# Kernel optimization log

Measured on AMD Instinct MI355X. Metric: run time of the kernel, lower is better.

Reference implementation:

```python
import jax, jax.numpy as jnp
import numpy as np

BZ, T, D, DFF, E, BEAMS = 128, 32, 768, 3072, 8, 2


def setup_inputs() -> dict:
    key = jax.random.key(0)
    ks = jax.random.split(key, 4)
    s = 0.02
    return {
        "x": jax.random.normal(ks[0], (BZ, T, D), jnp.float32),
        "attention_mask": jnp.ones((BZ, T), jnp.float32),
        "Wg": jax.random.normal(ks[1], (D, E), jnp.float32) * s,   # gate Linear(D,E,bias=False)
        "W1": jax.random.normal(ks[2], (E, D, DFF), jnp.float32) * s,
        "b1": jnp.zeros((E, DFF), jnp.float32),
        "W2": jax.random.normal(ks[3], (E, DFF, D), jnp.float32) * s,
        "b2": jnp.zeros((E, D), jnp.float32),
    }


def reference(x, attention_mask, Wg, W1, b1, W2, b2):
    # forward_gate: module builds its own all-ones mask regardless of input mask
    mask = jnp.ones((x.shape[0], x.shape[1]), x.dtype)
    x_avg = (x * mask[..., None]).sum(1) / mask[..., None].sum(1)   # [bz, D]
    prob = jax.nn.softmax(x_avg @ Wg, axis=-1)                       # [bz, E]
    # beam_search (layer_judge='first', pre-route): topk on exp(log(softmax)) == softmax probs
    scores = jnp.exp(jnp.log(prob))
    topv, topi = jax.lax.top_k(scores, BEAMS)                        # [bz, beams]
    beam_scores = topv.reshape(-1)                                   # [bz*beams]
    expert_route = topi.reshape(-1, 1)                                # [bz*beams, 1]
    sel = expert_route[:, -1]
    # replicate x per beam: [bz*beams, T, D]
    x_rep = jnp.broadcast_to(x[:, None], (x.shape[0], BEAMS, x.shape[1], x.shape[2]))
    x_rep = x_rep.reshape(-1, x.shape[1], x.shape[2])
    # per-sample expert FFN dispatch (dense masked loop over the E=8 experts)
    out = jnp.zeros_like(x_rep)
    for e in range(E):
        h = jax.nn.gelu(jnp.einsum('nsd,df->nsf', x_rep, W1[e]) + b1[e], approximate=False)
        ye = jnp.einsum('nsf,fd->nsd', h, W2[e]) + b2[e]
        out = jnp.where((sel == e)[:, None, None], ye, out)
    return (out, beam_scores, expert_route)
```

## Files before the change

### kernel.cpp

```cpp
#include <hip/hip_runtime.h>
#include <cstddef>
#include <cstdint>

#define BZd   128
#define Td    32
#define Dd    768
#define DFFd  3072
#define Ed    8
#define NBEAM 256
#define ROWS_TOT 8192
#define OUT_ELEMS 6291456
#define MAXTILES 72
#define MAXT2    40

typedef unsigned short u16;
typedef __attribute__((ext_vector_type(4))) unsigned short ushort4v;
typedef __attribute__((ext_vector_type(8))) short frag_ab;
typedef __attribute__((ext_vector_type(4))) float floatx4;

__device__ __forceinline__ u16 f2bf(float f) {
  unsigned int u = __builtin_bit_cast(unsigned int, f);
  u += 0x7FFFu + ((u >> 16) & 1u);
  return (u16)(u >> 16);
}

__device__ __forceinline__ void async_copy16(u16* lds, const u16* g) {
  __builtin_amdgcn_global_load_lds(
      (const __attribute__((address_space(1))) void*)g,
      (__attribute__((address_space(3))) void*)lds, 16, 0, 0);
}

__device__ __forceinline__ float gelu_fast(float x) {
  float z = 1.5957691216f * (x + 0.044715f * x * x * x);
  return x / (1.0f + __expf(-z));
}

__global__ __launch_bounds__(256) void route_kernel(
    const float* __restrict__ x, const float* __restrict__ Wg,
    float* __restrict__ out, int* __restrict__ sel) {
  int b = blockIdx.x;
  int t = threadIdx.x;
  __shared__ float red[256][8];
  float la[8];
#pragma unroll
  for (int e = 0; e < 8; e++) la[e] = 0.f;
  for (int d = t; d < Dd; d += 256) {
    const float* xp = x + (size_t)b * Td * Dd + d;
    float xa = 0.f;
#pragma unroll
    for (int tt = 0; tt < Td; tt++) xa += xp[(size_t)tt * Dd];
    xa *= (1.0f / 32.0f);
#pragma unroll
    for (int e = 0; e < 8; e++) la[e] += xa * Wg[d * 8 + e];
  }
#pragma unroll
  for (int e = 0; e < 8; e++) red[t][e] = la[e];
  __syncthreads();
  for (int s = 128; s > 0; s >>= 1) {
    if (t < s) {
#pragma unroll
      for (int e = 0; e < 8; e++) red[t][e] += red[t + s][e];
    }
    __syncthreads();
  }
  if (t == 0) {
    float lg[8];
#pragma unroll
    for (int e = 0; e < 8; e++) lg[e] = red[0][e];
    float mx = lg[0];
#pragma unroll
    for (int e = 1; e < 8; e++) mx = fmaxf(mx, lg[e]);
    float p[8];
    float sum = 0.f;
#pragma unroll
    for (int e = 0; e < 8; e++) { p[e] = __expf(lg[e] - mx); sum += p[e]; }
    float inv = 1.0f / sum;
#pragma unroll
    for (int e = 0; e < 8; e++) p[e] *= inv;
    int i0 = 0; float v0 = p[0];
#pragma unroll
    for (int e = 1; e < 8; e++) if (p[e] > v0) { v0 = p[e]; i0 = e; }
    int i1 = -1; float v1 = -1.0f;
#pragma unroll
    for (int e = 0; e < 8; e++) if (e != i0 && p[e] > v1) { v1 = p[e]; i1 = e; }
    float* bs = out + OUT_ELEMS;
    float* er = out + OUT_ELEMS + NBEAM;
    bs[2 * b] = v0; bs[2 * b + 1] = v1;
    er[2 * b] = (float)i0; er[2 * b + 1] = (float)i1;
    sel[2 * b] = i0; sel[2 * b + 1] = i1;
  }
}

__global__ __launch_bounds__(256) void bucket_kernel(
    const int* __restrict__ sel, int* __restrict__ perm,
    int4* __restrict__ tiles, int4* __restrict__ tiles2) {
  __shared__ int ssel[NBEAM];
  __shared__ int scnt[8];
  __shared__ int soff[8];
  __shared__ int scur[8];
  __shared__ int sperm[NBEAM];
  int t = threadIdx.x;
  ssel[t] = sel[t];
  __syncthreads();
  if (t == 0) {
    for (int e = 0; e < 8; e++) scnt[e] = 0;
    for (int n = 0; n < NBEAM; n++) scnt[ssel[n]]++;
    int o = 0;
    for (int e = 0; e < 8; e++) { soff[e] = o; scur[e] = o; o += scnt[e]; }
    for (int n = 0; n < NBEAM; n++) { int e = ssel[n]; sperm[scur[e]++] = n; }
    int tt = 0;
    for (int e = 0; e < 8; e++) {
      int nr = scnt[e] * 32;
      int base = soff[e] * 32;
      for (int r0 = 0; r0 < nr; r0 += 128) {
        tiles[tt] = make_int4(e, base + r0, min(128, nr - r0), 0);
        tt++;
      }
    }
    for (; tt < MAXTILES; tt++) tiles[tt] = make_int4(-1, 0, 0, 0);
    int t2 = 0;
    for (int e = 0; e < 8; e++) {
      int nr = scnt[e] * 32;
      int base = soff[e] * 32;
      for (int r0 = 0; r0 < nr; r0 += 256) {
        tiles2[t2] = make_int4(e, base + r0, min(256, nr - r0), 0);
        t2++;
      }
    }
    for (; t2 < MAXT2; t2++) tiles2[t2] = make_int4(-1, 0, 0, 0);
  }
  __syncthreads();
  perm[t] = sperm[t];
}

__global__ __launch_bounds__(256) void convert_x_kernel(
    const float* __restrict__ x, u16* __restrict__ xbf) {
  size_t i = ((size_t)blockIdx.x * 256 + threadIdx.x) * 4;
  float4 v = *(const float4*)(x + i);
  ushort4v pv = {f2bf(v.x), f2bf(v.y), f2bf(v.z), f2bf(v.w)};
  *(ushort4v*)(xbf + i) = pv;
}

__global__ __launch_bounds__(256) void transpose_bf16_kernel(
    const float* __restrict__ in, u16* __restrict__ out, int row0, int col0,
    int ld_in, size_t estr_in, int ld_out, size_t estr_out) {
  __shared__ u16 tile[64][65];
  int e = blockIdx.z;
  int r0 = blockIdx.x * 64, c0 = blockIdx.y * 64;
  int t = threadIdx.x;
  int rr = t >> 4, cc4 = (t & 15) * 4;
  const float* ip = in + (size_t)e * estr_in + (size_t)(row0 + r0) * ld_in + col0 + c0;
#pragma unroll
  for (int i = 0; i < 4; i++) {
    int r = rr + 16 * i;
    float4 v = *(const float4*)(ip + (size_t)r * ld_in + cc4);
    tile[r][cc4 + 0] = f2bf(v.x);
    tile[r][cc4 + 1] = f2bf(v.y);
    tile[r][cc4 + 2] = f2bf(v.z);
    tile[r][cc4 + 3] = f2bf(v.w);
  }
  __syncthreads();
  int ccw = t >> 4, r4 = (t & 15) * 4;
  u16* op = out + (size_t)e * estr_out + (size_t)c0 * ld_out + r0;
#pragma unroll
  for (int i = 0; i < 4; i++) {
    int cc = ccw + 16 * i;
    ushort4v pv = {tile[r4 + 0][cc], tile[r4 + 1][cc], tile[r4 + 2][cc], tile[r4 + 3][cc]};
    *(ushort4v*)(op + (size_t)cc * ld_out + r4) = pv;
  }
}

__global__ __launch_bounds__(512, 2) void gemm1_kernel(
    const u16* __restrict__ xbf, const u16* __restrict__ w1t,
    const float* __restrict__ b1, const int* __restrict__ perm,
    const int4* __restrict__ tiles2, u16* __restrict__ h, int f0, int FC) {
  int4 meta = tiles2[blockIdx.y];
  int e = meta.x;
  if (e < 0) return;
  int grow0 = meta.y, nrows = meta.z;
  int bx = blockIdx.x;

  extern __shared__ __align__(16) u16 smem[];
  u16* As = smem;
  u16* Bs = smem + 32768;

  int t = threadIdx.x;
  int l = t & 63;
  int wid = t >> 6;
  int wr = wid >> 2;
  int wc = wid & 3;
  int lrow = l & 15, lquad = l >> 4;

  const u16* ag[4]; const u16* bg[4];
  int ldst[4];
#pragma unroll
  for (int j = 0; j < 4; j++) {
    int s = j * 512 + t;
    int m = s >> 3;
    int koff = ((s & 7) ^ ((m >> 1) & 7)) * 8;
    int gr = grow0 + m;
    int bidx = gr >> 5; bidx = bidx < NBEAM ? bidx : NBEAM - 1;
    int batch = perm[bidx] >> 1;
    ag[j] = xbf + ((size_t)batch * Td + (m & 31)) * Dd + koff;
    bg[j] = w1t + ((size_t)e * FC + bx * 256 + m) * Dd + koff;
    ldst[j] = j * 4096 + t * 8;
  }

  int swz = (lrow >> 1) & 7;
  int ca0 = (lquad ^ swz) * 8, ca1 = ((lquad + 4) ^ swz) * 8;
  int abase0 = (wr * 128 + lrow) * 64 + ca0;
  int abase1 = (wr * 128 + lrow) * 64 + ca1;
  int bbase0 = (wc * 64 + lrow) * 64 + ca0;
  int bbase1 = (wc * 64 + lrow) * 64 + ca1;

  floatx4 acc[8][4];
#pragma unroll
  for (int mi = 0; mi < 8; mi++)
#pragma unroll
    for (int ni = 0; ni < 4; ni++) acc[mi][ni] = (floatx4){0.f, 0.f, 0.f, 0.f};

  const int nk = Dd / 64;

#pragma unroll
  for (int j = 0; j < 4; j++) { async_copy16(As + ldst[j], ag[j]); ag[j] += 64; }
#pragma unroll
  for (int j = 0; j < 4; j++) { async_copy16(Bs + ldst[j], bg[j]); bg[j] += 64; }

  for (int kt = 0; kt < nk; kt++) {
    const int b = kt & 1;
    const u16* Ab = As + b * 16384;
    const u16* Bb = Bs + b * 16384;
    const int pd = (b ^ 1) * 16384;
    const bool pre = (kt + 1 < nk);

    frag_ab af[4], bfr[4];

    if (pre) {
      async_copy16(As + pd + ldst[0], ag[0]); ag[0] += 64;
      async_copy16(As + pd + ldst[1], ag[1]); ag[1] += 64;
      asm volatile("s_waitcnt vmcnt(2)\n\ts_barrier" ::: "memory");
    } else {
      asm volatile("s_waitcnt vmcnt(0)\n\ts_barrier" ::: "memory");
    }
#pragma unroll
    for (int i = 0; i < 4; i++) bfr[i] = *(const frag_ab*)(Bb + bbase0 + i * 1024);
#pragma unroll
    for (int i = 0; i < 4; i++) af[i] = *(const frag_ab*)(Ab + abase0 + i * 1024);
    __builtin_amdgcn_s_setprio(1);
#pragma unroll
    for (int mi = 0; mi < 4; mi++)
#pragma unroll
      for (int ni = 0; ni < 4; ni++)
        acc[mi][ni] = __builtin_amdgcn_mfma_f32_16x16x32_bf16(bfr[ni], af[mi], acc[mi][ni], 0, 0, 0);
    __builtin_amdgcn_s_setprio(0);

    if (pre) {
      async_copy16(As + pd + ldst[2], ag[2]); ag[2] += 64;
      async_copy16(As + pd + ldst[3], ag[3]); ag[3] += 64;
    }
#pragma unroll
    for (int i = 0; i < 4; i++) af[i] = *(const frag_ab*)(Ab + abase0 + (i + 4) * 1024);
    __builtin_amdgcn_s_setprio(1);
#pragma unroll
    for (int mi = 0; mi < 4; mi++)
#pragma unroll
      for (int ni = 0; ni < 4; ni++)
        acc[mi + 4][ni] = __builtin_amdgcn_mfma_f32_16x16x32_bf16(bfr[ni], af[mi], acc[mi + 4][ni], 0, 0, 0);
    __builtin_amdgcn_s_setprio(0);

    if (pre) {
      async_copy16(Bs + pd + ldst[0], bg[0]); bg[0] += 64;
      async_copy16(Bs + pd + ldst[1], bg[1]); bg[1] += 64;
    }
#pragma unroll
    for (int i = 0; i < 4; i++) bfr[i] = *(const frag_ab*)(Bb + bbase1 + i * 1024);
#pragma unroll
    for (int i = 0; i < 4; i++) af[i] = *(const frag_ab*)(Ab + abase1 + i * 1024);
    __builtin_amdgcn_s_setprio(1);
#pragma unroll
    for (int mi = 0; mi < 4; mi++)
#pragma unroll
      for (int ni = 0; ni < 4; ni++)
        acc[mi][ni] = __builtin_amdgcn_mfma_f32_16x16x32_bf16(bfr[ni], af[mi], acc[mi][ni], 0, 0, 0);
    __builtin_amdgcn_s_setprio(0);

    if (pre) {
      async_copy16(Bs + pd + ldst[2], bg[2]); bg[2] += 64;
      async_copy16(Bs + pd + ldst[3], bg[3]); bg[3] += 64;
    }
#pragma unroll
    for (int i = 0; i < 4; i++) af[i] = *(const frag_ab*)(Ab + abase1 + (i + 4) * 1024);
    __builtin_amdgcn_s_setprio(1);
#pragma unroll
    for (int mi = 0; mi < 4; mi++)
#pragma unroll
      for (int ni = 0; ni < 4; ni++)
        acc[mi + 4][ni] = __builtin_amdgcn_mfma_f32_16x16x32_bf16(bfr[ni], af[mi], acc[mi + 4][ni], 0, 0, 0);
    __builtin_amdgcn_s_setprio(0);

    asm volatile("s_barrier" ::: "memory");
  }

#pragma unroll
  for (int mi = 0; mi < 8; mi++) {
    int row = wr * 128 + mi * 16 + lrow;
    if (row < nrows) {
      u16* hp = h + (size_t)(grow0 + row) * FC + bx * 256 + wc * 64 + lquad * 4;
      const float* bp = b1 + (size_t)e * DFFd + f0 + bx * 256 + wc * 64 + lquad * 4;
#pragma unroll
      for (int ni = 0; ni < 4; ni++) {
        float4 bias = *(const float4*)(bp + ni * 16);
        ushort4v pv = {f2bf(gelu_fast(acc[mi][ni][0] + bias.x)),
                       f2bf(gelu_fast(acc[mi][ni][1] + bias.y)),
                       f2bf(gelu_fast(acc[mi][ni][2] + bias.z)),
                       f2bf(gelu_fast(acc[mi][ni][3] + bias.w))};
        *(ushort4v*)(hp + ni * 16) = pv;
      }
    }
  }
}

__global__ __launch_bounds__(512, 2) void gemm2_kernel(
    const u16* __restrict__ h, const u16* __restrict__ w2t,
    const float* __restrict__ b2, const int* __restrict__ perm,
    const int4* __restrict__ tiles2, float* __restrict__ out,
    int FC, int first) {
  int4 meta = tiles2[blockIdx.y];
  int e = meta.x;
  if (e < 0) return;
  int grow0 = meta.y, nrows = meta.z;
  int bx = blockIdx.x;

  extern __shared__ __align__(16) u16 smem[];
  u16* As = smem;
  u16* Bs = smem + 32768;
  __shared__ int sbeam[8];

  int t = threadIdx.x;
  if (t < 8) {
    int idx = (grow0 >> 5) + t;
    sbeam[t] = perm[idx < NBEAM ? idx : NBEAM - 1];
  }
  __syncthreads();

  int l = t & 63;
  int wid = t >> 6;
  int wr = wid >> 2;
  int wc = wid & 3;
  int lrow = l & 15, lquad = l >> 4;

  const u16* ag[4]; const u16* bg[4];
  int ldst[4];
#pragma unroll
  for (int j = 0; j < 4; j++) {
    int s = j * 512 + t;
    int m = s >> 3;
    int koff = ((s & 7) ^ ((m >> 1) & 7)) * 8;
    int arow = grow0 + m;
    arow = arow < ROWS_TOT ? arow : ROWS_TOT - 1;
    ag[j] = h + (size_t)arow * FC + koff;
    bg[j] = w2t + ((size_t)e * Dd + bx * 256 + m) * FC + koff;
    ldst[j] = j * 4096 + t * 8;
  }

  int swz = (lrow >> 1) & 7;
  int ca0 = (lquad ^ swz) * 8, ca1 = ((lquad + 4) ^ swz) * 8;
  int abase0 = (wr * 128 + lrow) * 64 + ca0;
  int abase1 = (wr * 128 + lrow) * 64 + ca1;
  int bbase0 = (wc * 64 + lrow) * 64 + ca0;
  int bbase1 = (wc * 64 + lrow) * 64 + ca1;

  floatx4 acc[8][4];
#pragma unroll
  for (int mi = 0; mi < 8; mi++)
#pragma unroll
    for (int ni = 0; ni < 4; ni++) acc[mi][ni] = (floatx4){0.f, 0.f, 0.f, 0.f};

  const int nk = FC / 64;

#pragma unroll
  for (int j = 0; j < 4; j++) { async_copy16(As + ldst[j], ag[j]); ag[j] += 64; }
#pragma unroll
  for (int j = 0; j < 4; j++) { async_copy16(Bs + ldst[j], bg[j]); bg[j] += 64; }

  for (int kt = 0; kt < nk; kt++) {
    const int b = kt & 1;
    const u16* Ab = As + b * 16384;
    const u16* Bb = Bs + b * 16384;
    const int pd = (b ^ 1) * 16384;
    const bool pre = (kt + 1 < nk);

    frag_ab af[4], bfr[4];

    if (pre) {
      async_copy16(As + pd + ldst[0], ag[0]); ag[0] += 64;
      async_copy16(As + pd + ldst[1], ag[1]); ag[1] += 64;
      asm volatile("s_waitcnt vmcnt(2)\n\ts_barrier" ::: "memory");
    } else {
      asm volatile("s_waitcnt vmcnt(0)\n\ts_barrier" ::: "memory");
    }
#pragma unroll
    for (int i = 0; i < 4; i++) bfr[i] = *(const frag_ab*)(Bb + bbase0 + i * 1024);
#pragma unroll
    for (int i = 0; i < 4; i++) af[i] = *(const frag_ab*)(Ab + abase0 + i * 1024);
    __builtin_amdgcn_s_setprio(1);
#pragma unroll
    for (int mi = 0; mi < 4; mi++)
#pragma unroll
      for (int ni = 0; ni < 4; ni++)
        acc[mi][ni] = __builtin_amdgcn_mfma_f32_16x16x32_bf16(bfr[ni], af[mi], acc[mi][ni], 0, 0, 0);
    __builtin_amdgcn_s_setprio(0);

    if (pre) {
      async_copy16(As + pd + ldst[2], ag[2]); ag[2] += 64;
      async_copy16(As + pd + ldst[3], ag[3]); ag[3] += 64;
    }
#pragma unroll
    for (int i = 0; i < 4; i++) af[i] = *(const frag_ab*)(Ab + abase0 + (i + 4) * 1024);
    __builtin_amdgcn_s_setprio(1);
#pragma unroll
    for (int mi = 0; mi < 4; mi++)
#pragma unroll
      for (int ni = 0; ni < 4; ni++)
        acc[mi + 4][ni] = __builtin_amdgcn_mfma_f32_16x16x32_bf16(bfr[ni], af[mi], acc[mi + 4][ni], 0, 0, 0);
    __builtin_amdgcn_s_setprio(0);

    if (pre) {
      async_copy16(Bs + pd + ldst[0], bg[0]); bg[0] += 64;
      async_copy16(Bs + pd + ldst[1], bg[1]); bg[1] += 64;
    }
#pragma unroll
    for (int i = 0; i < 4; i++) bfr[i] = *(const frag_ab*)(Bb + bbase1 + i * 1024);
#pragma unroll
    for (int i = 0; i < 4; i++) af[i] = *(const frag_ab*)(Ab + abase1 + i * 1024);
    __builtin_amdgcn_s_setprio(1);
#pragma unroll
    for (int mi = 0; mi < 4; mi++)
#pragma unroll
      for (int ni = 0; ni < 4; ni++)
        acc[mi][ni] = __builtin_amdgcn_mfma_f32_16x16x32_bf16(bfr[ni], af[mi], acc[mi][ni], 0, 0, 0);
    __builtin_amdgcn_s_setprio(0);

    if (pre) {
      async_copy16(Bs + pd + ldst[2], bg[2]); bg[2] += 64;
      async_copy16(Bs + pd + ldst[3], bg[3]); bg[3] += 64;
    }
#pragma unroll
    for (int i = 0; i < 4; i++) af[i] = *(const frag_ab*)(Ab + abase1 + (i + 4) * 1024);
    __builtin_amdgcn_s_setprio(1);
#pragma unroll
    for (int mi = 0; mi < 4; mi++)
#pragma unroll
      for (int ni = 0; ni < 4; ni++)
        acc[mi + 4][ni] = __builtin_amdgcn_mfma_f32_16x16x32_bf16(bfr[ni], af[mi], acc[mi + 4][ni], 0, 0, 0);
    __builtin_amdgcn_s_setprio(0);

    asm volatile("s_barrier" ::: "memory");
  }

#pragma unroll
  for (int mi = 0; mi < 8; mi++) {
    int row = wr * 128 + mi * 16 + lrow;
    if (row < nrows) {
      int beam = sbeam[row >> 5];
      float* op = out + ((size_t)beam * Td + (row & 31)) * Dd + bx * 256 + wc * 64 + lquad * 4;
      const float* bp = b2 + (size_t)e * Dd + bx * 256 + wc * 64 + lquad * 4;
#pragma unroll
      for (int ni = 0; ni < 4; ni++) {
        if (first) {
          float4 bias = *(const float4*)(bp + ni * 16);
          float4 v = {acc[mi][ni][0] + bias.x, acc[mi][ni][1] + bias.y,
                      acc[mi][ni][2] + bias.z, acc[mi][ni][3] + bias.w};
          *(float4*)(op + ni * 16) = v;
        } else {
          float4 o = *(float4*)(op + ni * 16);
          o.x += acc[mi][ni][0]; o.y += acc[mi][ni][1];
          o.z += acc[mi][ni][2]; o.w += acc[mi][ni][3];
          *(float4*)(op + ni * 16) = o;
        }
      }
    }
  }
}

extern "C" void kernel_launch(void* const* d_in, const int* in_sizes, int n_in,
                              void* d_out, int out_size, void* d_ws, size_t ws_size,
                              hipStream_t stream) {
  const float* x  = (const float*)d_in[0];
  const float* Wg = (const float*)d_in[2];
  const float* W1 = (const float*)d_in[3];
  const float* b1 = (const float*)d_in[4];
  const float* W2 = (const float*)d_in[5];
  const float* b2 = (const float*)d_in[6];
  float* out = (float*)d_out;

  char* ws = (char*)d_ws;
  int*  sel    = (int*)ws;
  int*  perm   = sel + NBEAM;
  int4* tiles  = (int4*)(ws + 4096);
  int4* tiles2 = (int4*)(ws + 6144);

  const size_t xbf_off = 65536;
  const size_t xbf_bytes = (size_t)BZd * Td * Dd * 2;
  int FC = 768;
  if      (xbf_off + xbf_bytes + (size_t)40960 * 3072 <= ws_size) FC = 3072;
  else if (xbf_off + xbf_bytes + (size_t)40960 * 1536 <= ws_size) FC = 1536;
  int NC = DFFd / FC;

  u16* xbf = (u16*)(ws + xbf_off);
  u16* w1t = (u16*)(ws + xbf_off + xbf_bytes);
  u16* w2t = w1t + (size_t)Ed * FC * Dd;
  u16* h   = w2t + (size_t)Ed * Dd * FC;

  static bool attr_done = false;
  if (!attr_done) {
    hipFuncSetAttribute(reinterpret_cast<const void*>(gemm1_kernel),
                        hipFuncAttributeMaxDynamicSharedMemorySize, 131072);
    hipFuncSetAttribute(reinterpret_cast<const void*>(gemm2_kernel),
                        hipFuncAttributeMaxDynamicSharedMemorySize, 131072);
    attr_done = true;
  }

  route_kernel<<<BZd, 256, 0, stream>>>(x, Wg, out, sel);
  bucket_kernel<<<1, 256, 0, stream>>>(sel, perm, tiles, tiles2);
  convert_x_kernel<<<(BZd * Td * Dd) / 1024, 256, 0, stream>>>(x, xbf);

  for (int c = 0; c < NC; c++) {
    transpose_bf16_kernel<<<dim3(Dd / 64, FC / 64, Ed), 256, 0, stream>>>(
        W1, w1t, 0, c * FC, DFFd, (size_t)Dd * DFFd, Dd, (size_t)FC * Dd);
    transpose_bf16_kernel<<<dim3(FC / 64, Dd / 64, Ed), 256, 0, stream>>>(
        W2, w2t, c * FC, 0, Dd, (size_t)DFFd * Dd, FC, (size_t)Dd * FC);
    gemm1_kernel<<<dim3(FC / 256, MAXT2), 512, 131072, stream>>>(
        xbf, w1t, b1, perm, tiles2, h, c * FC, FC);
    gemm2_kernel<<<dim3(Dd / 256, MAXT2), 512, 131072, stream>>>(
        h, w2t, b2, perm, tiles2, out, FC, c == 0 ? 1 : 0);
  }
}
```

Before: 377.0 us.

## Split-K gemm2 over two slices with atomic accumulation and bias prefill in routing

Splits the second expert GEMM's reduction dimension into two halves along a new grid z dimension, doubling the number of workgroups, and accumulates results into the output with per-element float atomicAdd. The routing kernel now prefills the output with each beam's selected expert bias b2, so gemm2 no longer needs a first-chunk store path. The aim is to fix under-occupancy of the GPU, since gemm2 previously launched only 3 x 40 blocks. The cost is many scalar atomics to global memory, an extra full-output write in the routing kernel, and a summation order that is no longer deterministic.

```diff
diff --git a/kernel.cpp b/kernel.cpp
--- a/kernel.cpp
+++ b/kernel.cpp
@@ -37,10 +37,12 @@
 
 __global__ __launch_bounds__(256) void route_kernel(
     const float* __restrict__ x, const float* __restrict__ Wg,
-    float* __restrict__ out, int* __restrict__ sel) {
+    const float* __restrict__ b2, float* __restrict__ out,
+    int* __restrict__ sel) {
   int b = blockIdx.x;
   int t = threadIdx.x;
   __shared__ float red[256][8];
+  __shared__ int se2[2];
   float la[8];
 #pragma unroll
   for (int e = 0; e < 8; e++) la[e] = 0.f;
@@ -88,6 +90,17 @@
     bs[2 * b] = v0; bs[2 * b + 1] = v1;
     er[2 * b] = (float)i0; er[2 * b + 1] = (float)i1;
     sel[2 * b] = i0; sel[2 * b + 1] = i1;
+    se2[0] = i0; se2[1] = i1;
+  }
+  __syncthreads();
+#pragma unroll
+  for (int bm = 0; bm < 2; bm++) {
+    const float* brow = b2 + (size_t)se2[bm] * Dd;
+    float* orow = out + (size_t)(2 * b + bm) * Td * Dd;
+    for (int i = t; i < Td * Dd / 4; i += 256) {
+      float4 v = *(const float4*)(brow + (i % (Dd / 4)) * 4);
+      *(float4*)(orow + (size_t)i * 4) = v;
+    }
   }
 }
 
@@ -322,14 +335,15 @@
 
 __global__ __launch_bounds__(512, 2) void gemm2_kernel(
     const u16* __restrict__ h, const u16* __restrict__ w2t,
-    const float* __restrict__ b2, const int* __restrict__ perm,
-    const int4* __restrict__ tiles2, float* __restrict__ out,
-    int FC, int first) {
+    const int* __restrict__ perm, const int4* __restrict__ tiles2,
+    float* __restrict__ out, int FC) {
   int4 meta = tiles2[blockIdx.y];
   int e = meta.x;
   if (e < 0) return;
   int grow0 = meta.y, nrows = meta.z;
   int bx = blockIdx.x;
+  int kz = blockIdx.z;
+  const int KC = FC >> 1;
 
   extern __shared__ __align__(16) u16 smem[];
   u16* As = smem;
@@ -358,8 +372,8 @@
     int koff = ((s & 7) ^ ((m >> 1) & 7)) * 8;
     int arow = grow0 + m;
     arow = arow < ROWS_TOT ? arow : ROWS_TOT - 1;
-    ag[j] = h + (size_t)arow * FC + koff;
-    bg[j] = w2t + ((size_t)e * Dd + bx * 256 + m) * FC + koff;
+    ag[j] = h + (size_t)arow * FC + kz * KC + koff;
+    bg[j] = w2t + ((size_t)e * Dd + bx * 256 + m) * FC + kz * KC + koff;
     ldst[j] = j * 4096 + t * 8;
   }
 
@@ -376,7 +390,7 @@
 #pragma unroll
     for (int ni = 0; ni < 4; ni++) acc[mi][ni] = (floatx4){0.f, 0.f, 0.f, 0.f};
 
-  const int nk = FC / 64;
+  const int nk = KC / 64;
 
 #pragma unroll
   for (int j = 0; j < 4; j++) { async_copy16(As + ldst[j], ag[j]); ag[j] += 64; }
@@ -464,20 +478,11 @@
     if (row < nrows) {
       int beam = sbeam[row >> 5];
       float* op = out + ((size_t)beam * Td + (row & 31)) * Dd + bx * 256 + wc * 64 + lquad * 4;
-      const float* bp = b2 + (size_t)e * Dd + bx * 256 + wc * 64 + lquad * 4;
 #pragma unroll
       for (int ni = 0; ni < 4; ni++) {
-        if (first) {
-          float4 bias = *(const float4*)(bp + ni * 16);
-          float4 v = {acc[mi][ni][0] + bias.x, acc[mi][ni][1] + bias.y,
-                      acc[mi][ni][2] + bias.z, acc[mi][ni][3] + bias.w};
-          *(float4*)(op + ni * 16) = v;
-        } else {
-          float4 o = *(float4*)(op + ni * 16);
-          o.x += acc[mi][ni][0]; o.y += acc[mi][ni][1];
-          o.z += acc[mi][ni][2]; o.w += acc[mi][ni][3];
-          *(float4*)(op + ni * 16) = o;
-        }
+#pragma unroll
+        for (int jj = 0; jj < 4; jj++)
+          atomicAdd(op + ni * 16 + jj, acc[mi][ni][jj]);
       }
     }
   }
@@ -521,7 +526,7 @@
     attr_done = true;
   }
 
-  route_kernel<<<BZd, 256, 0, stream>>>(x, Wg, out, sel);
+  route_kernel<<<BZd, 256, 0, stream>>>(x, Wg, b2, out, sel);
   bucket_kernel<<<1, 256, 0, stream>>>(sel, perm, tiles, tiles2);
   convert_x_kernel<<<(BZd * Td * Dd) / 1024, 256, 0, stream>>>(x, xbf);
 
@@ -532,7 +537,7 @@
         W2, w2t, c * FC, 0, Dd, (size_t)DFFd * Dd, FC, (size_t)Dd * FC);
     gemm1_kernel<<<dim3(FC / 256, MAXT2), 512, 131072, stream>>>(
         xbf, w1t, b1, perm, tiles2, h, c * FC, FC);
-    gemm2_kernel<<<dim3(Dd / 256, MAXT2), 512, 131072, stream>>>(
-        h, w2t, b2, perm, tiles2, out, FC, c == 0 ? 1 : 0);
-  }
-}
+    gemm2_kernel<<<dim3(Dd / 256, MAXT2, 2), 512, 131072, stream>>>(
+        h, w2t, perm, tiles2, out, FC);
+  }
+}
```

Result: slower. 513.0 us (+36.1%).

## Split K dimension of second expert GEMM with partial buffer and reduce

Applied to the files above, without the earlier changes.

The second expert GEMM gets a z grid dimension of 2 when workspace allows. Each half of the K range writes its own fp32 result: the first half, with bias, goes to the output and the second to a workspace partial buffer. A separate reduce kernel then adds the two. The aim is to double the block count from 120 to fill a large-CU device, at the cost of extra partial-buffer writes and an elementwise reduction pass over the whole output.

```diff
diff --git a/kernel.cpp b/kernel.cpp
--- a/kernel.cpp
+++ b/kernel.cpp
@@ -324,12 +324,14 @@
     const u16* __restrict__ h, const u16* __restrict__ w2t,
     const float* __restrict__ b2, const int* __restrict__ perm,
     const int4* __restrict__ tiles2, float* __restrict__ out,
-    int FC, int first) {
+    float* __restrict__ part, int FC, int first) {
   int4 meta = tiles2[blockIdx.y];
   int e = meta.x;
   if (e < 0) return;
   int grow0 = meta.y, nrows = meta.z;
   int bx = blockIdx.x;
+  int kz = blockIdx.z;
+  const int KC = FC / (int)gridDim.z;
 
   extern __shared__ __align__(16) u16 smem[];
   u16* As = smem;
@@ -358,8 +360,8 @@
     int koff = ((s & 7) ^ ((m >> 1) & 7)) * 8;
     int arow = grow0 + m;
     arow = arow < ROWS_TOT ? arow : ROWS_TOT - 1;
-    ag[j] = h + (size_t)arow * FC + koff;
-    bg[j] = w2t + ((size_t)e * Dd + bx * 256 + m) * FC + koff;
+    ag[j] = h + (size_t)arow * FC + kz * KC + koff;
+    bg[j] = w2t + ((size_t)e * Dd + bx * 256 + m) * FC + kz * KC + koff;
     ldst[j] = j * 4096 + t * 8;
   }
 
@@ -376,7 +378,7 @@
 #pragma unroll
     for (int ni = 0; ni < 4; ni++) acc[mi][ni] = (floatx4){0.f, 0.f, 0.f, 0.f};
 
-  const int nk = FC / 64;
+  const int nk = KC / 64;
 
 #pragma unroll
   for (int j = 0; j < 4; j++) { async_copy16(As + ldst[j], ag[j]); ag[j] += 64; }
@@ -463,14 +465,17 @@
     int row = wr * 128 + mi * 16 + lrow;
     if (row < nrows) {
       int beam = sbeam[row >> 5];
-      float* op = out + ((size_t)beam * Td + (row & 31)) * Dd + bx * 256 + wc * 64 + lquad * 4;
+      size_t base = ((size_t)beam * Td + (row & 31)) * Dd + bx * 256 + wc * 64 + lquad * 4;
+      float* op = (kz == 0 ? out : part) + base;
       const float* bp = b2 + (size_t)e * Dd + bx * 256 + wc * 64 + lquad * 4;
 #pragma unroll
       for (int ni = 0; ni < 4; ni++) {
         if (first) {
-          float4 bias = *(const float4*)(bp + ni * 16);
-          float4 v = {acc[mi][ni][0] + bias.x, acc[mi][ni][1] + bias.y,
-                      acc[mi][ni][2] + bias.z, acc[mi][ni][3] + bias.w};
+          float4 v = {acc[mi][ni][0], acc[mi][ni][1], acc[mi][ni][2], acc[mi][ni][3]};
+          if (kz == 0) {
+            float4 bias = *(const float4*)(bp + ni * 16);
+            v.x += bias.x; v.y += bias.y; v.z += bias.z; v.w += bias.w;
+          }
           *(float4*)(op + ni * 16) = v;
         } else {
           float4 o = *(float4*)(op + ni * 16);
@@ -481,6 +486,15 @@
       }
     }
   }
+}
+
+__global__ __launch_bounds__(256) void reduce_kernel(
+    float* __restrict__ out, const float* __restrict__ part) {
+  size_t i = ((size_t)blockIdx.x * 256 + threadIdx.x) * 4;
+  float4 o = *(float4*)(out + i);
+  float4 p = *(const float4*)(part + i);
+  o.x += p.x; o.y += p.y; o.z += p.z; o.w += p.w;
+  *(float4*)(out + i) = o;
 }
 
 extern "C" void kernel_launch(void* const* d_in, const int* in_sizes, int n_in,
@@ -512,6 +526,11 @@
   u16* w2t = w1t + (size_t)Ed * FC * Dd;
   u16* h   = w2t + (size_t)Ed * Dd * FC;
 
+  const size_t part_off = xbf_off + xbf_bytes + (size_t)40960 * FC;
+  const size_t part_bytes = (size_t)OUT_ELEMS * 4;
+  int SPLIT = (part_off + part_bytes <= ws_size) ? 2 : 1;
+  float* part = (float*)(ws + part_off);
+
   static bool attr_done = false;
   if (!attr_done) {
     hipFuncSetAttribute(reinterpret_cast<const void*>(gemm1_kernel),
@@ -532,7 +551,9 @@
         W2, w2t, c * FC, 0, Dd, (size_t)DFFd * Dd, FC, (size_t)Dd * FC);
     gemm1_kernel<<<dim3(FC / 256, MAXT2), 512, 131072, stream>>>(
         xbf, w1t, b1, perm, tiles2, h, c * FC, FC);
-    gemm2_kernel<<<dim3(Dd / 256, MAXT2), 512, 131072, stream>>>(
-        h, w2t, b2, perm, tiles2, out, FC, c == 0 ? 1 : 0);
-  }
-}
+    gemm2_kernel<<<dim3(Dd / 256, MAXT2, SPLIT), 512, 131072, stream>>>(
+        h, w2t, b2, perm, tiles2, out, part, FC, c == 0 ? 1 : 0);
+  }
+  if (SPLIT == 2)
+    reduce_kernel<<<OUT_ELEMS / 1024, 256, 0, stream>>>(out, part);
+}
```

Result: no change. 371.7 us (-1.4%).
